# Kernel optimization log

Hardware: AMD Instinct MI355X
Metric: run time of the kernel (lower is better)

The kernel has to match this reference:

```python
import jax, jax.numpy as jnp
import numpy as np

N = 50000        # nodes
E = 800000       # edges (avg degree 16)
HID = 256        # hidden_size
HEADS = 8        # num_heads
HD = HID // HEADS  # head_dim = 32


def setup_inputs() -> dict:
    key = jax.random.key(0)
    ks = jax.random.split(key, 10)
    h = jax.random.normal(ks[0], (N, HID), dtype=jnp.float32)
    val = jax.random.uniform(ks[1], (E,), dtype=jnp.float32)
    Wq = jax.random.normal(ks[2], (HID, HID), dtype=jnp.float32) * 0.02
    Wk = jax.random.normal(ks[3], (HID, HID), dtype=jnp.float32) * 0.02
    Wv = jax.random.normal(ks[4], (HID, HID), dtype=jnp.float32) * 0.02
    bq = jnp.zeros((HID,), dtype=jnp.float32)
    bk = jnp.zeros((HID,), dtype=jnp.float32)
    bv = jnp.zeros((HID,), dtype=jnp.float32)
    # CSR rows expanded to per-edge row ids (sorted, like row_ptr expansion)
    edge_rows = jnp.sort(jax.random.randint(ks[5], (E,), 0, N, dtype=jnp.int32))
    col_ind = jax.random.randint(ks[6], (E,), 0, N, dtype=jnp.int32)
    return {"h": h, "val": val, "Wq": Wq, "bq": bq, "Wk": Wk, "bk": bk,
            "Wv": Wv, "bv": bv, "edge_rows": edge_rows, "col_ind": col_ind}


def reference(h, val, Wq, bq, Wk, bk, Wv, bv, edge_rows, col_ind):
    scaling = HD ** (-0.5)
    # projections; reshape splits hidden as (head_dim, heads) with heads fastest,
    # exactly as in the torch module: reshape(N, head_dim, num_heads)
    q = ((h @ Wq + bq).reshape(N, HD, HEADS)) * scaling
    k = (h @ Wk + bk).reshape(N, HD, HEADS)
    v = (h @ Wv + bv).reshape(N, HD, HEADS)

    # SDDMM restricted to edges: score[e, head] = <q[row_e], k[col_e]> * A.val[e]
    score = jnp.einsum('edh,edh->eh', q[edge_rows], k[col_ind]) * val[:, None]  # [E, HEADS]

    # per-destination-row softmax over incident edges (stable, segment ops)
    m = jax.ops.segment_max(score, edge_rows, num_segments=N)        # [N, HEADS]
    m = jnp.where(jnp.isfinite(m), m, jnp.zeros_like(m))             # empty rows
    e = jnp.exp(score - m[edge_rows])                                # [E, HEADS]
    denom = jax.ops.segment_sum(e, edge_rows, num_segments=N)        # [N, HEADS]
    attn = e / denom[edge_rows]

    # SpMM: out[i] = sum over edges (i, j) of attn * v[j]
    contrib = attn[:, None, :] * v[col_ind]                          # [E, HD, HEADS]
    out = jax.ops.segment_sum(contrib, edge_rows, num_segments=N)    # [N, HD, HEADS]
    return out.reshape(N, -1)                                        # [N, HID]
```

## Files before the change

### kernel.cpp

```cpp
#include <hip/hip_runtime.h>
#include <hip/hip_bf16.h>
#include <math.h>

static constexpr int kN   = 50000;
static constexpr int kE   = 800000;
static constexpr int kHID = 256;
static constexpr int kHD  = 32;

typedef short bf16x8 __attribute__((ext_vector_type(8)));
typedef float f32x4  __attribute__((ext_vector_type(4)));

__device__ __forceinline__ float b2f(unsigned short u) {
  union { unsigned v; float f; } c; c.v = ((unsigned)u) << 16; return c.f;
}

__device__ __forceinline__ unsigned short f2bu(float f) {
  __hip_bfloat16 b = __float2bfloat16(f);
  union { __hip_bfloat16 b; unsigned short u; } c; c.b = b; return c.u;
}

__device__ __forceinline__ void load_lds16(const void* g, void* l) {
  __builtin_amdgcn_global_load_lds(
      (const __attribute__((address_space(1))) unsigned int*)(unsigned long long)(uintptr_t)g,
      (__attribute__((address_space(3))) unsigned int*)(unsigned int)(uintptr_t)l,
      16, 0, 0);
}

__global__ void split_h_kernel(const float* __restrict__ h,
                               __hip_bfloat16* __restrict__ Ah) {
  int idx = blockIdx.x * 256 + threadIdx.x;
  Ah[idx] = __float2bfloat16(h[idx]);
}

__global__ void build_bt_kernel(const float* __restrict__ Wq, const float* __restrict__ bq,
                                const float* __restrict__ Wk, const float* __restrict__ bk,
                                const float* __restrict__ Wv, const float* __restrict__ bv,
                                __hip_bfloat16* __restrict__ Bt, float* __restrict__ biasP) {
  const int n  = blockIdx.x;
  const int kk = threadIdx.x;
  const int g  = n >> 8;
  const int cc = n & 255;
  const int c  = ((cc & 31) << 3) + (cc >> 5);
  const float scale = (g == 0) ? 0.17677669529663689f : 1.0f;
  const float* W = (g == 0) ? Wq : ((g == 1) ? Wk : Wv);
  Bt[n * 256 + kk] = __float2bfloat16(W[kk * 256 + c] * scale);
  if (kk == 0) {
    const float* b = (g == 0) ? bq : ((g == 1) ? bk : bv);
    biasP[n] = b[c] * scale;
  }
}

__global__ void build_row_ptr(const int* __restrict__ er, int* __restrict__ rp) {
  int i = blockIdx.x * blockDim.x + threadIdx.x;
  if (i > kN) return;
  int lo = 0, hi = kE;
  while (lo < hi) {
    int mid = (lo + hi) >> 1;
    if (er[mid] < i) lo = mid + 1; else hi = mid;
  }
  rp[i] = lo;
}

__global__ __launch_bounds__(256) void gemm_qkv_kernel(
    const __hip_bfloat16* __restrict__ Ah,
    const __hip_bfloat16* __restrict__ Bt, const float* __restrict__ biasP,
    __hip_bfloat16* __restrict__ qb, __hip_bfloat16* __restrict__ kvb) {
  __shared__ __align__(16) char smemRaw[34816];
  short* smemA = (short*)smemRaw;
  short* smemB = (short*)(smemRaw + 16384);
  short* smemC = (short*)smemRaw;

  const int tid  = threadIdx.x;
  const int wave = tid >> 6;
  const int lane = tid & 63;
  const int wm = wave & 1;
  const int wn = wave >> 1;
  const int colBase = blockIdx.x * 128;
  const int rowBase = blockIdx.y * 128;

  f32x4 acc[4][4];
#pragma unroll
  for (int i = 0; i < 4; ++i)
#pragma unroll
    for (int j = 0; j < 4; ++j) acc[i][j] = f32x4{0.f, 0.f, 0.f, 0.f};

  for (int k0 = 0; k0 < 256; k0 += 64) {
    __syncthreads();
#pragma unroll
    for (int j = 0; j < 4; ++j) {
      int s = (wave * 4 + j) * 64 + lane;
      int r = s >> 3, cp = s & 7;
      int c = cp ^ (r & 7);
      int grow = rowBase + r;
      grow = grow < kN ? grow : kN - 1;
      const char* gp = (const char*)Ah + (size_t)grow * 512 + k0 * 2 + c * 16;
      load_lds16(gp, (char*)smemA + (wave * 4 + j) * 1024);
    }
#pragma unroll
    for (int j = 0; j < 4; ++j) {
      int s = (wave * 4 + j) * 64 + lane;
      int r = s >> 3, cp = s & 7;
      int c = cp ^ (r & 7);
      const char* gp = (const char*)Bt + (size_t)(colBase + r) * 512 + k0 * 2 + c * 16;
      load_lds16(gp, (char*)smemB + (wave * 4 + j) * 1024);
    }
    __syncthreads();

    const int rq = lane & 15, qd = lane >> 4;
#pragma unroll
    for (int ks = 0; ks < 2; ++ks) {
      bf16x8 af[4], bfr[4];
#pragma unroll
      for (int mi = 0; mi < 4; ++mi) {
        int r = wm * 64 + mi * 16 + rq;
        int c = (ks * 4 + qd) ^ (r & 7);
        af[mi] = *(const bf16x8*)&smemA[r * 64 + c * 8];
      }
#pragma unroll
      for (int nj = 0; nj < 4; ++nj) {
        int r = wn * 64 + nj * 16 + rq;
        int c = (ks * 4 + qd) ^ (r & 7);
        bfr[nj] = *(const bf16x8*)&smemB[r * 64 + c * 8];
      }
#pragma unroll
      for (int mi = 0; mi < 4; ++mi)
#pragma unroll
        for (int nj = 0; nj < 4; ++nj)
          acc[mi][nj] = __builtin_amdgcn_mfma_f32_16x16x32_bf16(
              af[mi], bfr[nj], acc[mi][nj], 0, 0, 0);
    }
  }

  __syncthreads();
#pragma unroll
  for (int nj = 0; nj < 4; ++nj) {
    const int cl = wn * 64 + nj * 16 + (lane & 15);
    const float bb = biasP[colBase + cl];
#pragma unroll
    for (int mi = 0; mi < 4; ++mi) {
      const int rl = wm * 64 + mi * 16 + (lane >> 4) * 4;
#pragma unroll
      for (int reg = 0; reg < 4; ++reg) {
        smemC[(rl + reg) * 136 + cl] = (short)f2bu(acc[mi][nj][reg] + bb);
      }
    }
  }
  __syncthreads();

  const int g = colBase >> 8;
#pragma unroll
  for (int it = 0; it < 8; ++it) {
    const int r   = it * 16 + (tid >> 4);
    const int c16 = tid & 15;
    const int row = rowBase + r;
    if (row < kN) {
      bf16x8 vls = *(const bf16x8*)&smemC[r * 136 + c16 * 8];
      const int cc = (colBase & 255) + c16 * 8;
      __hip_bfloat16* dst =
          (g == 0) ? (qb + (size_t)row * 256 + cc)
                   : (kvb + (size_t)row * 512 + (g == 2 ? 256 : 0) + cc);
      *(bf16x8*)dst = vls;
    }
  }
}

__global__ __launch_bounds__(256) void edge_attn_kernel(
    const __hip_bfloat16* __restrict__ qb, const __hip_bfloat16* __restrict__ kvb,
    const int* __restrict__ row_ptr, const int* __restrict__ col_ind,
    const float* __restrict__ val, float* __restrict__ out) {
  const int wave = threadIdx.x >> 6;
  const int lane = threadIdx.x & 63;
  const int row = blockIdx.x * 4 + wave;
  if (row >= kN) return;

  const int e0 = row_ptr[row];
  const int e1 = row_ptr[row + 1];

  const ushort4* q4  = (const ushort4*)qb;
  const ushort4* kv4 = (const ushort4*)kvb;

  const ushort4 qu = q4[(size_t)row * 64 + lane];
  const float qx = b2f(qu.x), qy = b2f(qu.y), qz = b2f(qu.z), qw = b2f(qu.w);

  float denom = 0.f;
  float ax = 0.f, ay = 0.f, az = 0.f, aw = 0.f;

  ushort4 kA{}, vA{}, kB{}, vB{};
  float wA = 0.f, wB = 0.f;
  if (e0 < e1) {
    int c = col_ind[e0];
    wA = val[e0];
    kA = kv4[(size_t)c * 128 + lane];
    vA = kv4[(size_t)c * 128 + 64 + lane];
    int eB = (e0 + 1 < e1) ? e0 + 1 : e1 - 1;
    c = col_ind[eB];
    wB = val[eB];
    kB = kv4[(size_t)c * 128 + lane];
    vB = kv4[(size_t)c * 128 + 64 + lane];
  }

  for (int e = e0; e < e1; ++e) {
    const ushort4 kc = kA, vc = vA;
    const float wc = wA;
    kA = kB; vA = vB; wA = wB;
    const int eN = (e + 2 < e1) ? e + 2 : e1 - 1;
    {
      const int c = col_ind[eN];
      wB = val[eN];
      kB = kv4[(size_t)c * 128 + lane];
      vB = kv4[(size_t)c * 128 + 64 + lane];
    }

    float s = qx * b2f(kc.x) + qy * b2f(kc.y) + qz * b2f(kc.z) + qw * b2f(kc.w);
    s += __shfl_xor(s, 1);
    s += __shfl_xor(s, 2);
    s += __shfl_xor(s, 4);
    s *= wc;

    const float p = __expf(s);
    denom += p;
    ax = fmaf(p, b2f(vc.x), ax);
    ay = fmaf(p, b2f(vc.y), ay);
    az = fmaf(p, b2f(vc.z), az);
    aw = fmaf(p, b2f(vc.w), aw);
  }

  const float inv = (denom > 0.f) ? (1.0f / denom) : 0.f;
  const int h = lane >> 3;
  const int d0 = lane & 7;
  float* o = out + (size_t)row * 256 + d0 * 32 + h;
  o[0]  = ax * inv;
  o[8]  = ay * inv;
  o[16] = az * inv;
  o[24] = aw * inv;
}

extern "C" void kernel_launch(void* const* d_in, const int* in_sizes, int n_in,
                              void* d_out, int out_size, void* d_ws, size_t ws_size,
                              hipStream_t stream) {
  const float* h   = (const float*)d_in[0];
  const float* val = (const float*)d_in[1];
  const float* Wq  = (const float*)d_in[2];
  const float* bq  = (const float*)d_in[3];
  const float* Wk  = (const float*)d_in[4];
  const float* bk  = (const float*)d_in[5];
  const float* Wv  = (const float*)d_in[6];
  const float* bv  = (const float*)d_in[7];
  const int* edge_rows = (const int*)d_in[8];
  const int* col_ind   = (const int*)d_in[9];
  float* out = (float*)d_out;

  char* ws = (char*)d_ws;
  __hip_bfloat16* Ah  = (__hip_bfloat16*)ws;                 ws += (size_t)kN * 256 * 2;
  __hip_bfloat16* Bt  = (__hip_bfloat16*)ws;                 ws += (size_t)768 * 256 * 2;
  float*          biasP = (float*)ws;                        ws += 768 * 4;
  __hip_bfloat16* qb  = (__hip_bfloat16*)ws;                 ws += (size_t)kN * 256 * 2;
  __hip_bfloat16* kvb = (__hip_bfloat16*)ws;                 ws += (size_t)kN * 512 * 2;
  int* row_ptr = (int*)ws;

  split_h_kernel<<<kN, 256, 0, stream>>>(h, Ah);
  build_bt_kernel<<<768, 256, 0, stream>>>(Wq, bq, Wk, bk, Wv, bv, Bt, biasP);
  build_row_ptr<<<(kN + 1 + 255) / 256, 256, 0, stream>>>(edge_rows, row_ptr);

  gemm_qkv_kernel<<<dim3(6, 391), 256, 0, stream>>>(Ah, Bt, biasP, qb, kvb);

  edge_attn_kernel<<<(kN + 3) / 4, 256, 0, stream>>>(qb, kvb, row_ptr, col_ind,
                                                     val, out);
}
```

Before: 292.6 us.

## Process two edges per wave with half-waves and 16-byte vector loads

Each wave now splits into two 32-lane halves, and each half handles alternating edges of the row. Each lane loads 8 bf16 values (16 bytes) of k and v instead of 4, so a half-wave covers a full 256-wide row and two edges are in flight per iteration. The per-lane accumulators are combined across halves with shuffles at the end. This is meant to raise the memory-level parallelism of the gather and halve the number of loop iterations. The cost is more registers and wasted lanes when a row has an odd edge count.

```diff
diff --git a/kernel.cpp b/kernel.cpp
--- a/kernel.cpp
+++ b/kernel.cpp
@@ -9,6 +9,7 @@
 
 typedef short bf16x8 __attribute__((ext_vector_type(8)));
 typedef float f32x4  __attribute__((ext_vector_type(4)));
+typedef unsigned short us8 __attribute__((ext_vector_type(8)));
 
 __device__ __forceinline__ float b2f(unsigned short u) {
   union { unsigned v; float f; } c; c.v = ((unsigned)u) << 16; return c.f;
@@ -170,69 +171,78 @@
     const float* __restrict__ val, float* __restrict__ out) {
   const int wave = threadIdx.x >> 6;
   const int lane = threadIdx.x & 63;
+  const int half = lane >> 5;
+  const int sl   = lane & 31;
   const int row = blockIdx.x * 4 + wave;
   if (row >= kN) return;
 
   const int e0 = row_ptr[row];
   const int e1 = row_ptr[row + 1];
 
-  const ushort4* q4  = (const ushort4*)qb;
-  const ushort4* kv4 = (const ushort4*)kvb;
-
-  const ushort4 qu = q4[(size_t)row * 64 + lane];
-  const float qx = b2f(qu.x), qy = b2f(qu.y), qz = b2f(qu.z), qw = b2f(qu.w);
+  const us8 qu = *(const us8*)(qb + (size_t)row * 256 + sl * 8);
+  float qf[8];
+#pragma unroll
+  for (int j = 0; j < 8; ++j) qf[j] = b2f(qu[j]);
 
   float denom = 0.f;
-  float ax = 0.f, ay = 0.f, az = 0.f, aw = 0.f;
-
-  ushort4 kA{}, vA{}, kB{}, vB{};
-  float wA = 0.f, wB = 0.f;
+  float acc[8];
+#pragma unroll
+  for (int j = 0; j < 8; ++j) acc[j] = 0.f;
+
   if (e0 < e1) {
-    int c = col_ind[e0];
-    wA = val[e0];
-    kA = kv4[(size_t)c * 128 + lane];
-    vA = kv4[(size_t)c * 128 + 64 + lane];
-    int eB = (e0 + 1 < e1) ? e0 + 1 : e1 - 1;
-    c = col_ind[eB];
-    wB = val[eB];
-    kB = kv4[(size_t)c * 128 + lane];
-    vB = kv4[(size_t)c * 128 + 64 + lane];
-  }
-
-  for (int e = e0; e < e1; ++e) {
-    const ushort4 kc = kA, vc = vA;
-    const float wc = wA;
-    kA = kB; vA = vB; wA = wB;
-    const int eN = (e + 2 < e1) ? e + 2 : e1 - 1;
+    us8 kA, vA, kB, vB;
+    float wA, wB;
     {
-      const int c = col_ind[eN];
-      wB = val[eN];
-      kB = kv4[(size_t)c * 128 + lane];
-      vB = kv4[(size_t)c * 128 + 64 + lane];
-    }
-
-    float s = qx * b2f(kc.x) + qy * b2f(kc.y) + qz * b2f(kc.z) + qw * b2f(kc.w);
-    s += __shfl_xor(s, 1);
-    s += __shfl_xor(s, 2);
-    s += __shfl_xor(s, 4);
-    s *= wc;
-
-    const float p = __expf(s);
-    denom += p;
-    ax = fmaf(p, b2f(vc.x), ax);
-    ay = fmaf(p, b2f(vc.y), ay);
-    az = fmaf(p, b2f(vc.z), az);
-    aw = fmaf(p, b2f(vc.w), aw);
-  }
+      const int eh = min(e0 + half, e1 - 1);
+      const int c = col_ind[eh];
+      wA = val[eh];
+      kA = *(const us8*)(kvb + (size_t)c * 512 + sl * 8);
+      vA = *(const us8*)(kvb + (size_t)c * 512 + 256 + sl * 8);
+      const int eh2 = min(e0 + 2 + half, e1 - 1);
+      const int c2 = col_ind[eh2];
+      wB = val[eh2];
+      kB = *(const us8*)(kvb + (size_t)c2 * 512 + sl * 8);
+      vB = *(const us8*)(kvb + (size_t)c2 * 512 + 256 + sl * 8);
+    }
+
+    for (int e = e0; e < e1; e += 2) {
+      const us8 kc = kA, vc = vA;
+      const float wc = wA;
+      kA = kB; vA = vB; wA = wB;
+      {
+        const int ehN = min(e + 4 + half, e1 - 1);
+        const int c = col_ind[ehN];
+        wB = val[ehN];
+        kB = *(const us8*)(kvb + (size_t)c * 512 + sl * 8);
+        vB = *(const us8*)(kvb + (size_t)c * 512 + 256 + sl * 8);
+      }
+
+      float s = 0.f;
+#pragma unroll
+      for (int j = 0; j < 8; ++j) s = fmaf(qf[j], b2f(kc[j]), s);
+      s += __shfl_xor(s, 1);
+      s += __shfl_xor(s, 2);
+      s *= wc;
+
+      float p = __expf(s);
+      p = ((e + half) < e1) ? p : 0.f;
+      denom += p;
+#pragma unroll
+      for (int j = 0; j < 8; ++j) acc[j] = fmaf(p, b2f(vc[j]), acc[j]);
+    }
+  }
+
+#pragma unroll
+  for (int j = 0; j < 8; ++j) acc[j] += __shfl_xor(acc[j], 32);
+  denom += __shfl_xor(denom, 32);
 
   const float inv = (denom > 0.f) ? (1.0f / denom) : 0.f;
-  const int h = lane >> 3;
-  const int d0 = lane & 7;
-  float* o = out + (size_t)row * 256 + d0 * 32 + h;
-  o[0]  = ax * inv;
-  o[8]  = ay * inv;
-  o[16] = az * inv;
-  o[24] = aw * inv;
+  const int h = sl >> 2;
+  const int dbase = (sl & 3) * 8 + half * 4;
+  float* o = out + (size_t)row * 256 + h;
+#pragma unroll
+  for (int jj = 0; jj < 4; ++jj)
+    o[(dbase + jj) * 8] = acc[half * 4 + jj] * inv;
 }
 
 extern "C" void kernel_launch(void* const* d_in, const int* in_sizes, int n_in,
```

Result: no change. 294.4 us (+0.6%).
